# Performance work log

Hardware: AMD Instinct MI355X
Metric: run time of the kernel (lower is better)

The kernel has to match this reference:

```python
import jax, jax.numpy as jnp
import numpy as np

HIDDEN = 512
N_LAYERS = 2
SEQ = 512
BATCH = 64
H2 = HIDDEN * 2  # 1024
D_IN = H2 * (N_LAYERS + 1)  # 3072


def setup_inputs() -> dict:
    key = jax.random.key(0)
    ks = jax.random.split(key, 4)
    state = jax.random.normal(ks[0], (N_LAYERS, BATCH, H2), dtype=jnp.float32)
    encoder_output = jax.random.normal(ks[1], (SEQ, BATCH, H2), dtype=jnp.float32)
    # fc1: xavier_normal with tanh gain (5/3); fc2: kaiming_normal
    xavier_std = (5.0 / 3.0) * np.sqrt(2.0 / (D_IN + H2))
    W1 = jax.random.normal(ks[2], (H2, D_IN), dtype=jnp.float32) * xavier_std
    b1 = jnp.zeros((H2,), dtype=jnp.float32)
    W2 = jax.random.normal(ks[3], (1, H2), dtype=jnp.float32) * np.sqrt(2.0 / H2)
    b2 = jnp.zeros((1,), dtype=jnp.float32)
    return {"state": state, "encoder_output": encoder_output,
            "W1": W1, "b1": b1, "W2": W2, "b2": b2}


def reference(state, encoder_output, W1, b1, W2, b2):
    S, B, h2 = encoder_output.shape
    # (n_layers, B, H2) -> (B, n_layers*H2), broadcast over seq
    st = jnp.transpose(state, (1, 0, 2)).reshape(B, -1)
    st = jnp.broadcast_to(st[:, None, :], (B, S, st.shape[-1]))
    enc = jnp.transpose(encoder_output, (1, 0, 2))  # (B, S, H2)
    concat = jnp.concatenate([st, enc], axis=2)      # (B, S, 3*H2)
    energy = jnp.tanh(jnp.einsum('bsd,hd->bsh', concat, W1) + b1)
    energy = (jnp.einsum('bsh,oh->bso', energy, W2) + b2)  # (B, S, 1)
    energy = jnp.transpose(energy, (0, 2, 1))        # (B, 1, S)
    alpha = jax.nn.softmax(energy, axis=2)           # (B, 1, S)
    context = jnp.einsum('bqs,bsh->qbh', alpha, enc)  # (1, B, H2)
    return context, alpha
```

## Files before the change

### kernel.cpp

```cpp
#include <hip/hip_runtime.h>
#include <hip/hip_bf16.h>
#include <stdint.h>

#define H2      1024
#define SEQ     512
#define BATCH   64
#define M_TOTAL (SEQ * BATCH)

typedef __attribute__((ext_vector_type(8))) short short8;
typedef __attribute__((ext_vector_type(4))) float f32x4;

__device__ __forceinline__ unsigned pack2_bf16(float lo, float hi) {
    union { __hip_bfloat162 h; unsigned u; } v;
    v.h = __float22bfloat162_rn(make_float2(lo, hi));
    return v.u;
}

__device__ __forceinline__ float fast_tanh(float x) {
    float e = __expf(2.0f * x);
    return __fdividef(e - 1.0f, e + 1.0f);
}

__device__ __forceinline__ void gl_lds16(const unsigned short* g, unsigned short* l) {
    __builtin_amdgcn_global_load_lds(
        (const __attribute__((address_space(1))) unsigned int*)g,
        (__attribute__((address_space(3))) unsigned int*)l, 16, 0, 0);
}

__global__ __launch_bounds__(256) void k_prep(const float* __restrict__ W1,
                                              unsigned short* __restrict__ W1e) {
    int i = blockIdx.x * 256 + threadIdx.x;
    int e = i << 2;
    int h = e >> 10, k = e & 1023;
    float4 v = *(const float4*)(W1 + (size_t)h * 3072 + 2048 + k);
    uint2 o;
    o.x = pack2_bf16(v.x, v.y);
    o.y = pack2_bf16(v.z, v.w);
    *(uint2*)(W1e + ((size_t)h << 10) + k) = o;
}

__global__ __launch_bounds__(256) void k_prep_enc(const float* __restrict__ enc,
                                                  unsigned short* __restrict__ encb) {
    size_t i = ((size_t)blockIdx.x * 256 + threadIdx.x) << 3;
    float4 v0 = *(const float4*)(enc + i);
    float4 v1 = *(const float4*)(enc + i + 4);
    uint4 o;
    o.x = pack2_bf16(v0.x, v0.y); o.y = pack2_bf16(v0.z, v0.w);
    o.z = pack2_bf16(v1.x, v1.y); o.w = pack2_bf16(v1.z, v1.w);
    *(uint4*)(encb + i) = o;
}

__global__ __launch_bounds__(256) void k_stateproj(const float* __restrict__ W1,
                                                   const float* __restrict__ state,
                                                   const float* __restrict__ b1,
                                                   float* __restrict__ sp) {
    int lane = threadIdx.x & 63;
    int wave = threadIdx.x >> 6;
    int mT   = blockIdx.x;
    int c    = lane & 15;
    int kq   = (lane >> 4) << 3;
    int h    = mT * 16 + c;
    int b    = wave * 16 + c;
    const float* ap = W1 + (size_t)h * 3072 + kq;
    f32x4 acc = {0.f, 0.f, 0.f, 0.f};
    #pragma unroll 4
    for (int k0 = 0; k0 < 2048; k0 += 32) {
        int k = k0 + kq;
        float4 a0 = *(const float4*)(ap + k0);
        float4 a1 = *(const float4*)(ap + k0 + 4);
        int l = k >> 10, j = k & 1023;
        const float* bp = state + (((size_t)l * 64 + b) << 10) + j;
        float4 b0 = *(const float4*)bp;
        float4 b1v = *(const float4*)(bp + 4);
        union { short8 s; uint4 u; } fa, fb;
        fa.u.x = pack2_bf16(a0.x, a0.y); fa.u.y = pack2_bf16(a0.z, a0.w);
        fa.u.z = pack2_bf16(a1.x, a1.y); fa.u.w = pack2_bf16(a1.z, a1.w);
        fb.u.x = pack2_bf16(b0.x, b0.y); fb.u.y = pack2_bf16(b0.z, b0.w);
        fb.u.z = pack2_bf16(b1v.x, b1v.y); fb.u.w = pack2_bf16(b1v.z, b1v.w);
        acc = __builtin_amdgcn_mfma_f32_16x16x32_bf16(fa.s, fb.s, acc, 0, 0, 0);
    }
    int quad = lane >> 4;
    int bcol = wave * 16 + c;
    #pragma unroll
    for (int i = 0; i < 4; ++i) {
        int hh = mT * 16 + quad * 4 + i;
        sp[((size_t)bcol << 10) + hh] = acc[i] + b1[hh];
    }
}

#define BM 128
#define BN 128
#define BK 32

__global__ __launch_bounds__(256, 2) void k_energy(const unsigned short* __restrict__ encb,
                                                   const unsigned short* __restrict__ W1e,
                                                   const float* __restrict__ sp,
                                                   const float* __restrict__ W2,
                                                   float* __restrict__ logits) {
    __shared__ unsigned short As[BM * BK];
    __shared__ unsigned short Bs[BN * BK];
    int bid = blockIdx.x;
    int c8  = bid & 7;
    int jj  = bid >> 3;
    int mT  = c8 * 32 + (jj >> 3);
    int nT  = jj & 7;
    int m0  = mT * BM, n0 = nT * BN;
    int tid  = threadIdx.x;
    int lane = tid & 63, wave = tid >> 6;
    int wm   = (wave >> 1) << 6;
    int wn   = (wave & 1) << 6;

    int r    = lane >> 2;
    int kk   = (lane & 3) << 3;
    int srow = wave * 32 + r;
    const unsigned short* gA = encb + (size_t)(m0 + srow) * H2 + kk;
    const unsigned short* gB = W1e  + (size_t)(n0 + srow) * H2 + kk;
    unsigned short* lA = As + srow * BK + kk;
    unsigned short* lB = Bs + srow * BK + kk;

    f32x4 acc[4][4];
    #pragma unroll
    for (int mi = 0; mi < 4; ++mi)
        #pragma unroll
        for (int ni = 0; ni < 4; ++ni)
            acc[mi][ni] = (f32x4){0.f, 0.f, 0.f, 0.f};

    int c  = lane & 15;
    int kq = (lane >> 4) << 3;
    const unsigned short* afp = As + (wm + c) * BK + kq;
    const unsigned short* bfp = Bs + (wn + c) * BK + kq;

    for (int k0 = 0; k0 < H2; k0 += BK) {
        __syncthreads();
        gl_lds16(gA + k0,           lA);
        gl_lds16(gA + 16 * H2 + k0, lA + 16 * BK);
        gl_lds16(gB + k0,           lB);
        gl_lds16(gB + 16 * H2 + k0, lB + 16 * BK);
        __syncthreads();
        short8 af[4], bf[4];
        #pragma unroll
        for (int i = 0; i < 4; ++i) {
            af[i] = *(const short8*)(afp + (i << 4) * BK);
            bf[i] = *(const short8*)(bfp + (i << 4) * BK);
        }
        #pragma unroll
        for (int mi = 0; mi < 4; ++mi)
            #pragma unroll
            for (int ni = 0; ni < 4; ++ni)
                acc[mi][ni] = __builtin_amdgcn_mfma_f32_16x16x32_bf16(af[mi], bf[ni], acc[mi][ni], 0, 0, 0);
    }

    int quad = lane >> 4;
    float w2v[4];
    int   hcol[4];
    #pragma unroll
    for (int ni = 0; ni < 4; ++ni) {
        hcol[ni] = n0 + wn + ni * 16 + c;
        w2v[ni]  = W2[hcol[ni]];
    }
    #pragma unroll
    for (int mi = 0; mi < 4; ++mi) {
        #pragma unroll
        for (int i = 0; i < 4; ++i) {
            int m = m0 + wm + mi * 16 + quad * 4 + i;
            int b = m & 63;
            const float* sprow = sp + ((size_t)b << 10);
            float t = 0.f;
            #pragma unroll
            for (int ni = 0; ni < 4; ++ni) {
                float e = acc[mi][ni][i] + sprow[hcol[ni]];
                t = fmaf(fast_tanh(e), w2v[ni], t);
            }
            t += __shfl_xor(t, 1);
            t += __shfl_xor(t, 2);
            t += __shfl_xor(t, 4);
            t += __shfl_xor(t, 8);
            if (c == 0) atomicAdd(logits + (size_t)b * 512 + (m >> 6), t);
        }
    }
}

#define LDT 40
__global__ __launch_bounds__(256, 2) void k_energy_f32(const float* __restrict__ enc,
                                                       const unsigned short* __restrict__ W1e,
                                                       const float* __restrict__ sp,
                                                       const float* __restrict__ W2,
                                                       float* __restrict__ logits) {
    __shared__ unsigned short As[BM * LDT];
    __shared__ unsigned short Bs[BN * LDT];
    int bid = blockIdx.x;
    int c8  = bid & 7;
    int jj  = bid >> 3;
    int mT  = c8 * 32 + (jj >> 3);
    int nT  = jj & 7;
    int tid  = threadIdx.x;
    int lane = tid & 63, wave = tid >> 6;
    int wm   = (wave >> 1) << 6;
    int wn   = (wave & 1) << 6;
    int m0   = mT * BM, n0 = nT * BN;

    int arow = tid >> 1;
    int aseg = (tid & 1) << 4;
    const float*          apg = enc + ((size_t)(m0 + arow) << 10) + aseg;
    const unsigned short* wpg = W1e + ((size_t)(n0 + arow) << 10) + aseg;
    unsigned short* asd = As + arow * LDT + aseg;
    unsigned short* bsd = Bs + arow * LDT + aseg;

    f32x4 acc[4][4];
    #pragma unroll
    for (int mi = 0; mi < 4; ++mi)
        #pragma unroll
        for (int ni = 0; ni < 4; ++ni)
            acc[mi][ni] = (f32x4){0.f, 0.f, 0.f, 0.f};

    int c  = lane & 15;
    int kq = (lane >> 4) << 3;
    const unsigned short* afp = As + (wm + c) * LDT + kq;
    const unsigned short* bfp = Bs + (wn + c) * LDT + kq;

    for (int k0 = 0; k0 < 1024; k0 += BK) {
        float4 a0 = *(const float4*)(apg + k0);
        float4 a1 = *(const float4*)(apg + k0 + 4);
        float4 a2 = *(const float4*)(apg + k0 + 8);
        float4 a3 = *(const float4*)(apg + k0 + 12);
        uint4  w0 = *(const uint4*)(wpg + k0);
        uint4  w1 = *(const uint4*)(wpg + k0 + 8);
        uint4 pa0, pa1;
        pa0.x = pack2_bf16(a0.x, a0.y); pa0.y = pack2_bf16(a0.z, a0.w);
        pa0.z = pack2_bf16(a1.x, a1.y); pa0.w = pack2_bf16(a1.z, a1.w);
        pa1.x = pack2_bf16(a2.x, a2.y); pa1.y = pack2_bf16(a2.z, a2.w);
        pa1.z = pack2_bf16(a3.x, a3.y); pa1.w = pack2_bf16(a3.z, a3.w);
        __syncthreads();
        *(uint4*)asd       = pa0;
        *(uint4*)(asd + 8) = pa1;
        *(uint4*)bsd       = w0;
        *(uint4*)(bsd + 8) = w1;
        __syncthreads();
        short8 af[4], bf[4];
        #pragma unroll
        for (int i = 0; i < 4; ++i) {
            af[i] = *(const short8*)(afp + (i << 4) * LDT);
            bf[i] = *(const short8*)(bfp + (i << 4) * LDT);
        }
        #pragma unroll
        for (int mi = 0; mi < 4; ++mi)
            #pragma unroll
            for (int ni = 0; ni < 4; ++ni)
                acc[mi][ni] = __builtin_amdgcn_mfma_f32_16x16x32_bf16(af[mi], bf[ni], acc[mi][ni], 0, 0, 0);
    }

    int quad = lane >> 4;
    float w2v[4];
    int   hcol[4];
    #pragma unroll
    for (int ni = 0; ni < 4; ++ni) {
        hcol[ni] = n0 + wn + ni * 16 + c;
        w2v[ni]  = W2[hcol[ni]];
    }
    #pragma unroll
    for (int mi = 0; mi < 4; ++mi) {
        #pragma unroll
        for (int i = 0; i < 4; ++i) {
            int m = m0 + wm + mi * 16 + quad * 4 + i;
            int b = m & 63;
            const float* sprow = sp + ((size_t)b << 10);
            float t = 0.f;
            #pragma unroll
            for (int ni = 0; ni < 4; ++ni) {
                float e = acc[mi][ni][i] + sprow[hcol[ni]];
                t = fmaf(fast_tanh(e), w2v[ni], t);
            }
            t += __shfl_xor(t, 1);
            t += __shfl_xor(t, 2);
            t += __shfl_xor(t, 4);
            t += __shfl_xor(t, 8);
            if (c == 0) atomicAdd(logits + (size_t)b * 512 + (m >> 6), t);
        }
    }
}

__global__ __launch_bounds__(256) void k_softmax(const float* __restrict__ logits,
                                                 float* __restrict__ alpha) {
    int b = blockIdx.x;
    int tid = threadIdx.x;
    int lane = tid & 63, wave = tid >> 6;
    float v0 = logits[(size_t)b * 512 + tid];
    float v1 = logits[(size_t)b * 512 + 256 + tid];
    float mx = fmaxf(v0, v1);
    #pragma unroll
    for (int o = 32; o; o >>= 1) mx = fmaxf(mx, __shfl_xor(mx, o));
    __shared__ float redm[4];
    if (lane == 0) redm[wave] = mx;
    __syncthreads();
    mx = fmaxf(fmaxf(redm[0], redm[1]), fmaxf(redm[2], redm[3]));
    float e0 = __expf(v0 - mx), e1 = __expf(v1 - mx);
    float s = e0 + e1;
    #pragma unroll
    for (int o = 32; o; o >>= 1) s += __shfl_xor(s, o);
    __shared__ float reds[4];
    if (lane == 0) reds[wave] = s;
    __syncthreads();
    s = reds[0] + reds[1] + reds[2] + reds[3];
    float inv = 1.0f / s;
    alpha[(size_t)b * 512 + tid]       = e0 * inv;
    alpha[(size_t)b * 512 + 256 + tid] = e1 * inv;
}

__global__ __launch_bounds__(256) void k_context(const float* __restrict__ enc,
                                                 const float* __restrict__ alpha,
                                                 float* __restrict__ ctx) {
    int b  = blockIdx.x & 63;
    int sc = blockIdx.x >> 6;
    int h  = threadIdx.x << 2;
    float4 acc = make_float4(0.f, 0.f, 0.f, 0.f);
    int sbase = sc * 64;
    #pragma unroll 4
    for (int si = 0; si < 64; ++si) {
        int s = sbase + si;
        float a = alpha[(size_t)b * 512 + s];
        float4 e = *(const float4*)(enc + (((size_t)s * 64 + b) << 10) + h);
        acc.x = fmaf(a, e.x, acc.x);
        acc.y = fmaf(a, e.y, acc.y);
        acc.z = fmaf(a, e.z, acc.z);
        acc.w = fmaf(a, e.w, acc.w);
    }
    float* dst = ctx + ((size_t)b << 10) + h;
    atomicAdd(dst + 0, acc.x);
    atomicAdd(dst + 1, acc.y);
    atomicAdd(dst + 2, acc.z);
    atomicAdd(dst + 3, acc.w);
}

extern "C" void kernel_launch(void* const* d_in, const int* in_sizes, int n_in,
                              void* d_out, int out_size, void* d_ws, size_t ws_size,
                              hipStream_t stream) {
    const float* state = (const float*)d_in[0];
    const float* enc   = (const float*)d_in[1];
    const float* W1    = (const float*)d_in[2];
    const float* b1    = (const float*)d_in[3];
    const float* W2    = (const float*)d_in[4];

    float* ctx   = (float*)d_out;
    float* alpha = (float*)d_out + 65536;

    char* ws = (char*)d_ws;
    unsigned short* W1e    = (unsigned short*)(ws);
    float*          sp     = (float*)(ws + 2097152);
    float*          logits = (float*)(ws + 2097152 + 262144);
    unsigned short* encb   = (unsigned short*)(ws + 2097152 + 262144 + 131072);

    const size_t need_full = 2097152 + 262144 + 131072 + (size_t)M_TOTAL * H2 * 2;

    hipMemsetAsync(logits, 0, 64 * 512 * sizeof(float), stream);
    hipMemsetAsync(ctx, 0, 65536 * sizeof(float), stream);
    k_prep<<<1024, 256, 0, stream>>>(W1, W1e);
    k_stateproj<<<64, 256, 0, stream>>>(W1, state, b1, sp);
    if (ws_size >= need_full) {
        k_prep_enc<<<16384, 256, 0, stream>>>(enc, encb);
        k_energy<<<M_TOTAL / BM * (H2 / BN), 256, 0, stream>>>(encb, W1e, sp, W2, logits);
    } else {
        k_energy_f32<<<M_TOTAL / BM * (H2 / BN), 256, 0, stream>>>(enc, W1e, sp, W2, logits);
    }
    k_softmax<<<64, 256, 0, stream>>>(logits, alpha);
    k_context<<<512, 256, 0, stream>>>(enc, alpha, ctx);
}
```

Baseline: 419.6 us.

## Deepen GEMM K tile with fragment-contiguous LDS layout and fold memsets into kernels

The energy GEMM now loads 64-wide K tiles into an LDS layout where each 16x32 fragment is contiguous, halving barrier count and avoiding strided LDS reads, and requests three blocks per CU. The memsets of logits and context are folded into the prep and softmax kernels, and the state projection is split by layer across twice as many blocks combined with atomics into a bias-initialized buffer. The tighter launch bound may raise register pressure, and atomic accumulation changes summation order.

```diff
diff --git a/kernel.cpp b/kernel.cpp
--- a/kernel.cpp
+++ b/kernel.cpp
@@ -28,8 +28,12 @@
 }
 
 __global__ __launch_bounds__(256) void k_prep(const float* __restrict__ W1,
-                                              unsigned short* __restrict__ W1e) {
-    int i = blockIdx.x * 256 + threadIdx.x;
+                                              const float* __restrict__ b1,
+                                              unsigned short* __restrict__ W1e,
+                                              float* __restrict__ logits,
+                                              float* __restrict__ sp) {
+    int blk = blockIdx.x, tid = threadIdx.x;
+    int i = blk * 256 + tid;
     int e = i << 2;
     int h = e >> 10, k = e & 1023;
     float4 v = *(const float4*)(W1 + (size_t)h * 3072 + 2048 + k);
@@ -37,6 +41,12 @@
     o.x = pack2_bf16(v.x, v.y);
     o.y = pack2_bf16(v.z, v.w);
     *(uint2*)(W1e + ((size_t)h << 10) + k) = o;
+    if (blk < 128) {
+        logits[i] = 0.f;
+    } else if (blk < 384) {
+        int j = i - 32768;
+        sp[j] = b1[j & 1023];
+    }
 }
 
 __global__ __launch_bounds__(256) void k_prep_enc(const float* __restrict__ enc,
@@ -52,26 +62,24 @@
 
 __global__ __launch_bounds__(256) void k_stateproj(const float* __restrict__ W1,
                                                    const float* __restrict__ state,
-                                                   const float* __restrict__ b1,
                                                    float* __restrict__ sp) {
     int lane = threadIdx.x & 63;
     int wave = threadIdx.x >> 6;
-    int mT   = blockIdx.x;
+    int blk  = blockIdx.x;
+    int mT   = blk >> 1, l = blk & 1;
     int c    = lane & 15;
     int kq   = (lane >> 4) << 3;
     int h    = mT * 16 + c;
     int b    = wave * 16 + c;
-    const float* ap = W1 + (size_t)h * 3072 + kq;
+    const float* ap = W1 + (size_t)h * 3072 + l * 1024 + kq;
+    const float* bp = state + (((size_t)l * 64 + b) << 10) + kq;
     f32x4 acc = {0.f, 0.f, 0.f, 0.f};
     #pragma unroll 4
-    for (int k0 = 0; k0 < 2048; k0 += 32) {
-        int k = k0 + kq;
+    for (int k0 = 0; k0 < 1024; k0 += 32) {
         float4 a0 = *(const float4*)(ap + k0);
         float4 a1 = *(const float4*)(ap + k0 + 4);
-        int l = k >> 10, j = k & 1023;
-        const float* bp = state + (((size_t)l * 64 + b) << 10) + j;
-        float4 b0 = *(const float4*)bp;
-        float4 b1v = *(const float4*)(bp + 4);
+        float4 b0 = *(const float4*)(bp + k0);
+        float4 b1v = *(const float4*)(bp + k0 + 4);
         union { short8 s; uint4 u; } fa, fb;
         fa.u.x = pack2_bf16(a0.x, a0.y); fa.u.y = pack2_bf16(a0.z, a0.w);
         fa.u.z = pack2_bf16(a1.x, a1.y); fa.u.w = pack2_bf16(a1.z, a1.w);
@@ -82,17 +90,15 @@
     int quad = lane >> 4;
     int bcol = wave * 16 + c;
     #pragma unroll
-    for (int i = 0; i < 4; ++i) {
-        int hh = mT * 16 + quad * 4 + i;
-        sp[((size_t)bcol << 10) + hh] = acc[i] + b1[hh];
-    }
+    for (int i = 0; i < 4; ++i)
+        atomicAdd(&sp[((size_t)bcol << 10) + mT * 16 + quad * 4 + i], acc[i]);
 }
 
 #define BM 128
 #define BN 128
-#define BK 32
-
-__global__ __launch_bounds__(256, 2) void k_energy(const unsigned short* __restrict__ encb,
+#define BK 64
+
+__global__ __launch_bounds__(256, 3) void k_energy(const unsigned short* __restrict__ encb,
                                                    const unsigned short* __restrict__ W1e,
                                                    const float* __restrict__ sp,
                                                    const float* __restrict__ W2,
@@ -110,13 +116,23 @@
     int wm   = (wave >> 1) << 6;
     int wn   = (wave & 1) << 6;
 
-    int r    = lane >> 2;
-    int kk   = (lane & 3) << 3;
-    int srow = wave * 32 + r;
-    const unsigned short* gA = encb + (size_t)(m0 + srow) * H2 + kk;
-    const unsigned short* gB = W1e  + (size_t)(n0 + srow) * H2 + kk;
-    unsigned short* lA = As + srow * BK + kk;
-    unsigned short* lB = Bs + srow * BK + kk;
+    int rowl = lane & 15;
+    int q    = lane >> 4;
+
+    const unsigned short* gA[4];
+    const unsigned short* gB[4];
+    unsigned short* lA[4];
+    unsigned short* lB[4];
+    #pragma unroll
+    for (int j = 0; j < 4; ++j) {
+        int r   = wave * 4 + j;
+        int Bb  = r >> 1, ssub = r & 1;
+        int kof = ssub * 32 + q * 8;
+        gA[j] = encb + (size_t)(m0 + Bb * 16 + rowl) * H2 + kof;
+        gB[j] = W1e  + (size_t)(n0 + Bb * 16 + rowl) * H2 + kof;
+        lA[j] = As + r * 512 + lane * 8;
+        lB[j] = Bs + r * 512 + lane * 8;
+    }
 
     f32x4 acc[4][4];
     #pragma unroll
@@ -125,31 +141,36 @@
         for (int ni = 0; ni < 4; ++ni)
             acc[mi][ni] = (f32x4){0.f, 0.f, 0.f, 0.f};
 
-    int c  = lane & 15;
-    int kq = (lane >> 4) << 3;
-    const unsigned short* afp = As + (wm + c) * BK + kq;
-    const unsigned short* bfp = Bs + (wn + c) * BK + kq;
+    const unsigned short* afb = As + lane * 8;
+    const unsigned short* bfb = Bs + lane * 8;
+    int ablk = (wm >> 4) * 2;
+    int bblk = (wn >> 4) * 2;
 
     for (int k0 = 0; k0 < H2; k0 += BK) {
         __syncthreads();
-        gl_lds16(gA + k0,           lA);
-        gl_lds16(gA + 16 * H2 + k0, lA + 16 * BK);
-        gl_lds16(gB + k0,           lB);
-        gl_lds16(gB + 16 * H2 + k0, lB + 16 * BK);
+        #pragma unroll
+        for (int j = 0; j < 4; ++j) {
+            gl_lds16(gA[j] + k0, lA[j]);
+            gl_lds16(gB[j] + k0, lB[j]);
+        }
         __syncthreads();
-        short8 af[4], bf[4];
-        #pragma unroll
-        for (int i = 0; i < 4; ++i) {
-            af[i] = *(const short8*)(afp + (i << 4) * BK);
-            bf[i] = *(const short8*)(bfp + (i << 4) * BK);
-        }
-        #pragma unroll
-        for (int mi = 0; mi < 4; ++mi)
-            #pragma unroll
-            for (int ni = 0; ni < 4; ++ni)
-                acc[mi][ni] = __builtin_amdgcn_mfma_f32_16x16x32_bf16(af[mi], bf[ni], acc[mi][ni], 0, 0, 0);
-    }
-
+        #pragma unroll
+        for (int s = 0; s < 2; ++s) {
+            short8 af[4], bf[4];
+            #pragma unroll
+            for (int i = 0; i < 4; ++i) {
+                af[i] = *(const short8*)(afb + (size_t)(ablk + i * 2 + s) * 512);
+                bf[i] = *(const short8*)(bfb + (size_t)(bblk + i * 2 + s) * 512);
+            }
+            #pragma unroll
+            for (int mi = 0; mi < 4; ++mi)
+                #pragma unroll
+                for (int ni = 0; ni < 4; ++ni)
+                    acc[mi][ni] = __builtin_amdgcn_mfma_f32_16x16x32_bf16(af[mi], bf[ni], acc[mi][ni], 0, 0, 0);
+        }
+    }
+
+    int c    = lane & 15;
     int quad = lane >> 4;
     float w2v[4];
     int   hcol[4];
@@ -218,7 +239,7 @@
     const unsigned short* afp = As + (wm + c) * LDT + kq;
     const unsigned short* bfp = Bs + (wn + c) * LDT + kq;
 
-    for (int k0 = 0; k0 < 1024; k0 += BK) {
+    for (int k0 = 0; k0 < 1024; k0 += 32) {
         float4 a0 = *(const float4*)(apg + k0);
         float4 a1 = *(const float4*)(apg + k0 + 4);
         float4 a2 = *(const float4*)(apg + k0 + 8);
@@ -280,10 +301,14 @@
 }
 
 __global__ __launch_bounds__(256) void k_softmax(const float* __restrict__ logits,
-                                                 float* __restrict__ alpha) {
+                                                 float* __restrict__ alpha,
+                                                 float* __restrict__ ctx) {
     int b = blockIdx.x;
     int tid = threadIdx.x;
     int lane = tid & 63, wave = tid >> 6;
+    #pragma unroll
+    for (int j = 0; j < 4; ++j)
+        ctx[((size_t)b << 10) + j * 256 + tid] = 0.f;
     float v0 = logits[(size_t)b * 512 + tid];
     float v1 = logits[(size_t)b * 512 + 256 + tid];
     float mx = fmaxf(v0, v1);
@@ -351,16 +376,14 @@
 
     const size_t need_full = 2097152 + 262144 + 131072 + (size_t)M_TOTAL * H2 * 2;
 
-    hipMemsetAsync(logits, 0, 64 * 512 * sizeof(float), stream);
-    hipMemsetAsync(ctx, 0, 65536 * sizeof(float), stream);
-    k_prep<<<1024, 256, 0, stream>>>(W1, W1e);
-    k_stateproj<<<64, 256, 0, stream>>>(W1, state, b1, sp);
+    k_prep<<<1024, 256, 0, stream>>>(W1, b1, W1e, logits, sp);
+    k_stateproj<<<128, 256, 0, stream>>>(W1, state, sp);
     if (ws_size >= need_full) {
         k_prep_enc<<<16384, 256, 0, stream>>>(enc, encb);
         k_energy<<<M_TOTAL / BM * (H2 / BN), 256, 0, stream>>>(encb, W1e, sp, W2, logits);
     } else {
         k_energy_f32<<<M_TOTAL / BM * (H2 / BN), 256, 0, stream>>>(enc, W1e, sp, W2, logits);
     }
-    k_softmax<<<64, 256, 0, stream>>>(logits, alpha);
+    k_softmax<<<64, 256, 0, stream>>>(logits, alpha, ctx);
     k_context<<<512, 256, 0, stream>>>(enc, alpha, ctx);
 }
```

Measured after the change: 431.8 us. +2.9%, slower.
